# Optimization experiments

Hardware: AMD Instinct MI355X
Metric: run time of the kernel (lower is better)

Reference implementation:

```python
import jax, jax.numpy as jnp
import numpy as np

K = 2048      # codebook_size
D = 64        # codebook_dim
B = 32
T = 4096
W = 0.99      # codebook_loss_weight (EMA decay)
THRESH = 1.0  # discard_vec_threshold


def setup_inputs() -> dict:
    key = jax.random.key(0)
    k1, k2 = jax.random.split(key, 2)
    x = jax.random.normal(k1, (B, D, T), jnp.float32)
    codebook = jax.random.normal(k2, (K, D), jnp.float32)
    codebook_avg = codebook.copy()
    vector_usage = jnp.ones((K,), jnp.float32)
    perm = jnp.arange(B * T, dtype=jnp.int32)  # deterministic stand-in for randperm
    return dict(x=x, codebook=codebook, codebook_avg=codebook_avg,
                vector_usage=vector_usage, perm=perm)


def reference(x, codebook, codebook_avg, vector_usage, perm):
    Bv, E, Tv = x.shape
    sg = jax.lax.stop_gradient
    # preprocess: [B, E, T] -> [N, E]
    xf = jnp.transpose(x, (0, 2, 1)).reshape(-1, E)
    N = xf.shape[0]
    x_norm = jnp.linalg.norm(xf - jnp.mean(xf)) / np.sqrt(N * E)
    # squared euclidean distances [N, K]
    d = (jnp.sum(xf * xf, axis=-1, keepdims=True)
         - 2.0 * (xf @ codebook.T)
         + jnp.sum(codebook * codebook, axis=-1))
    idx = jnp.argmin(d, axis=-1)            # [N]
    fit = jnp.mean(jnp.min(d, axis=-1))
    q = codebook[idx]                       # [N, E] gather
    # --- update_codebook (torch.no_grad) ---
    cb_sum = jax.ops.segment_sum(sg(xf), idx, num_segments=K)          # onehot @ x
    counts = jax.ops.segment_sum(jnp.ones((N,), xf.dtype), idx, num_segments=K)
    new_avg = W * sg(codebook_avg) + (1.0 - W) * cb_sum
    new_usage = W * sg(vector_usage) + (1.0 - W) * counts
    keep = (new_usage >= THRESH).astype(xf.dtype)[:, None]
    random_shift = sg(xf)[perm][:K]
    new_codebook = keep * (new_avg / new_usage[:, None]) + (1.0 - keep) * random_shift
    vector_prob = counts / jnp.sum(counts)
    entropy = -jnp.sum(vector_prob * jnp.log(vector_prob + 1e-8))
    codebook_diff = jnp.linalg.norm(new_codebook - sg(codebook)) / np.sqrt(K * E)
    # --- commitment loss + straight-through ---
    commit_loss = jnp.sum((sg(q) - xf) ** 2) / (N * E)
    out = xf + sg(q - xf)
    out = jnp.transpose(out.reshape(Bv, Tv, E), (0, 2, 1))  # [B, E, T]
    return (out, commit_loss, fit, x_norm, new_codebook, new_avg, new_usage,
            entropy, codebook_diff)
```

## Files before the change

kernel.cpp:

```cpp
#include <hip/hip_runtime.h>
#include <math.h>

#define OUT_X      0
#define OUT_COMMIT 8388608
#define OUT_FIT    8388609
#define OUT_XNORM  8388610
#define OUT_NCB    8388611
#define OUT_NAVG   (8388611 + 131072)
#define OUT_NUSE   (8388611 + 262144)
#define OUT_ENT    (8388611 + 264192)
#define OUT_CBDIFF (8388611 + 264193)

#define WS_DACC    0
#define WS_COUNTS  64
#define WS_CBSUM   8256
#define WS_CURS    532544
#define WS_XN2     540736
#define WS_IDX     1065024
#define WS_CN2H    1589312
#define WS_SORTED  1597504
#define WS_CHI     2121792
#define WS_CLO     2383936
#define WS_ZERO_BYTES 532544

#define LO_SCALE5  32.0f

typedef _Float16 f16x8_t __attribute__((ext_vector_type(8)));
typedef float f32x16_t __attribute__((ext_vector_type(16)));

__device__ __forceinline__ void gload_lds16(const _Float16* g, _Float16* l) {
    __builtin_amdgcn_global_load_lds(
        (const __attribute__((address_space(1))) unsigned int*)(g),
        (__attribute__((address_space(3))) unsigned int*)(l), 16, 0, 0);
}

__global__ __launch_bounds__(256) void kern_prep_x(
    const float* __restrict__ x, float* __restrict__ xt,
    float* __restrict__ xn2, double* __restrict__ dacc)
{
    __shared__ __align__(16) float Xs[64][128];
    __shared__ float tmpA[4], tmpB[4];
    const int tid = threadIdx.x;
    const int n0 = blockIdx.x * 128;
    const int b = n0 >> 12, t0 = n0 & 4095;
    const float* xb = x + ((size_t)b << 18) + t0;
#pragma unroll
    for (int i = 0; i < 8; ++i) {
        int c = i * 256 + tid;
        int e = c >> 5, v4 = c & 31;
        float4 f = *(const float4*)(xb + ((size_t)e << 12) + (v4 << 2));
        *(float4*)&Xs[e][v4 << 2] = f;
    }
    __syncthreads();
    const int q = tid & 3, r0 = tid >> 2;
    float s1t = 0.f, s2t = 0.f;
#pragma unroll
    for (int h = 0; h < 2; ++h) {
        int r = r0 + (h << 6);
        float s2 = 0.f;
#pragma unroll
        for (int j = 0; j < 4; ++j) {
            int e = q * 16 + j * 4;
            float4 f = make_float4(Xs[e][r], Xs[e + 1][r], Xs[e + 2][r], Xs[e + 3][r]);
            *(float4*)(xt + (((size_t)(n0 + r)) << 6) + e) = f;
            s1t += f.x + f.y + f.z + f.w;
            s2 += f.x * f.x + f.y * f.y + f.z * f.z + f.w * f.w;
        }
        s2t += s2;
        float s2q = s2 + __shfl_xor(s2, 1, 64);
        s2q += __shfl_xor(s2q, 2, 64);
        if (q == 0) xn2[n0 + r] = s2q;
    }
    float rs = s1t, r2 = s2t;
#pragma unroll
    for (int m = 32; m >= 1; m >>= 1) {
        rs += __shfl_xor(rs, m, 64);
        r2 += __shfl_xor(r2, m, 64);
    }
    if ((tid & 63) == 0) { tmpA[tid >> 6] = rs; tmpB[tid >> 6] = r2; }
    __syncthreads();
    if (tid == 0) {
        atomicAdd(&dacc[0], (double)(tmpA[0] + tmpA[1] + tmpA[2] + tmpA[3]));
        atomicAdd(&dacc[1], (double)(tmpB[0] + tmpB[1] + tmpB[2] + tmpB[3]));
    }
}

__global__ __launch_bounds__(256) void kern_prep_cb(
    const float* __restrict__ cb, _Float16* __restrict__ chi,
    _Float16* __restrict__ clo, float* __restrict__ cn2h)
{
    __shared__ float Cs[128][68];
    const int tid = threadIdx.x;
    const int c0 = blockIdx.x * 128;
#pragma unroll
    for (int i = 0; i < 8; ++i) {
        int li = i * 256 + tid;
        int code = li >> 4, d4 = li & 15;
        float4 f = *(const float4*)(cb + (((size_t)(c0 + code)) << 6) + (d4 << 2));
        Cs[code][d4 * 4 + 0] = f.x; Cs[code][d4 * 4 + 1] = f.y;
        Cs[code][d4 * 4 + 2] = f.z; Cs[code][d4 * 4 + 3] = f.w;
    }
    __syncthreads();
    const int w = tid >> 6, lane = tid & 63;
    const int cl = (w << 5) + (lane & 31);
    const int g = lane >> 5;
    const int ktg = blockIdx.x * 4 + w;
#pragma unroll
    for (int s = 0; s < 4; ++s) {
        f16x8_t hh, ll;
#pragma unroll
        for (int i = 0; i < 8; ++i) {
            int k = 16 * s + 4 * g + (i & 3) + 8 * (i >> 2);
            float v = Cs[cl][k];
            _Float16 h = (_Float16)v;
            hh[i] = h;
            ll[i] = (_Float16)((v - (float)h) * LO_SCALE5);
        }
        *(f16x8_t*)(chi + (((size_t)(ktg * 4 + s)) << 9) + lane * 8) = hh;
        *(f16x8_t*)(clo + (((size_t)(ktg * 4 + s)) << 9) + lane * 8) = ll;
    }
    if (tid < 128) {
        float s = 0.f;
#pragma unroll
        for (int k = 0; k < 64; ++k) { float v = Cs[tid][k]; s = fmaf(v, v, s); }
        cn2h[c0 + tid] = -0.5f * s;
    }
}

__global__ __launch_bounds__(256, 2) void kern_argmin_mfma(
    const float* __restrict__ xt, const float* __restrict__ cn2h,
    const _Float16* __restrict__ chi, const _Float16* __restrict__ clo,
    const float* __restrict__ xn2, int* __restrict__ idxb,
    unsigned* __restrict__ counts, double* __restrict__ dacc)
{
    __shared__ __align__(16) _Float16 Bs[3][2][8][512];
    __shared__ float cvs[2048];
    const int tid = threadIdx.x;
    const int w = tid >> 6, lane = tid & 63;
    const int n0 = blockIdx.x * 256 + w * 64;
    const int l31 = lane & 31, g = lane >> 5;

    for (int i = tid; i < 2048; i += 256) cvs[i] = cn2h[i];

    f16x8_t ahi[2][4], alo5[2][4];
#pragma unroll
    for (int rb = 0; rb < 2; ++rb) {
        const float* xr = xt + ((size_t)(n0 + rb * 32 + l31) << 6) + 4 * g;
#pragma unroll
        for (int s = 0; s < 4; ++s) {
            float4 p = *(const float4*)(xr + 16 * s);
            float4 q = *(const float4*)(xr + 16 * s + 8);
            float vals[8] = {p.x, p.y, p.z, p.w, q.x, q.y, q.z, q.w};
#pragma unroll
            for (int i = 0; i < 8; ++i) {
                _Float16 h = (_Float16)vals[i];
                ahi[rb][s][i] = h;
                alo5[rb][s][i] = (_Float16)((vals[i] - (float)h) * LO_SCALE5);
            }
        }
    }
    float bestm[2][16]; int besti[2][16];
#pragma unroll
    for (int rb = 0; rb < 2; ++rb)
#pragma unroll
        for (int r = 0; r < 16; ++r) { bestm[rb][r] = -INFINITY; besti[rb][r] = 0; }

    __syncthreads();

#pragma unroll
    for (int kt = 0; kt < 2; ++kt)
#pragma unroll
        for (int j = 0; j < 4; ++j) {
            int seg = (j << 2) | w;
            int tt = seg >> 3, sh = seg & 7;
            const _Float16* src = ((sh & 1) ? clo : chi)
                + ((((size_t)(kt * 2 + tt)) * 4 + (sh >> 1)) << 9) + lane * 8;
            gload_lds16(src, &Bs[kt][tt][sh][0]);
        }

    int cur = 0, nxt = 2;
    for (int kt = 0; kt < 32; ++kt) {
        if (kt < 30) asm volatile("s_waitcnt vmcnt(4)" ::: "memory");
        else         asm volatile("s_waitcnt vmcnt(0)" ::: "memory");
        __builtin_amdgcn_s_barrier();
        if (kt + 2 < 32) {
#pragma unroll
            for (int j = 0; j < 4; ++j) {
                int seg = (j << 2) | w;
                int tt = seg >> 3, sh = seg & 7;
                const _Float16* src = ((sh & 1) ? clo : chi)
                    + ((((size_t)((kt + 2) * 2 + tt)) * 4 + (sh >> 1)) << 9) + lane * 8;
                gload_lds16(src, &Bs[nxt][tt][sh][0]);
            }
        }
#pragma unroll
        for (int tt = 0; tt < 2; ++tt) {
            const int tg = kt * 2 + tt;
            f16x8_t bh[4], bl[4];
#pragma unroll
            for (int s = 0; s < 4; ++s) {
                bh[s] = *(const f16x8_t*)&Bs[cur][tt][s * 2 + 0][lane * 8];
                bl[s] = *(const f16x8_t*)&Bs[cur][tt][s * 2 + 1][lane * 8];
            }
            float cv = cvs[(tg << 5) + l31];
            f32x16_t a0, a1;
#pragma unroll
            for (int r = 0; r < 16; ++r) { a0[r] = cv; a1[r] = cv; }
#pragma unroll
            for (int s = 0; s < 4; ++s) {
                a0 = __builtin_amdgcn_mfma_f32_32x32x16_f16(ahi[0][s], bh[s], a0, 0, 0, 0);
                a1 = __builtin_amdgcn_mfma_f32_32x32x16_f16(ahi[1][s], bh[s], a1, 0, 0, 0);
                f16x8_t bh5 = bh[s] * (_Float16)0.03125f;
                a0 = __builtin_amdgcn_mfma_f32_32x32x16_f16(alo5[0][s], bh5, a0, 0, 0, 0);
                a1 = __builtin_amdgcn_mfma_f32_32x32x16_f16(alo5[1][s], bh5, a1, 0, 0, 0);
                f16x8_t h50 = ahi[0][s] * (_Float16)0.03125f;
                f16x8_t h51 = ahi[1][s] * (_Float16)0.03125f;
                a0 = __builtin_amdgcn_mfma_f32_32x32x16_f16(h50, bl[s], a0, 0, 0, 0);
                a1 = __builtin_amdgcn_mfma_f32_32x32x16_f16(h51, bl[s], a1, 0, 0, 0);
            }
#pragma unroll
            for (int r = 0; r < 16; ++r) {
                if (a0[r] > bestm[0][r]) { bestm[0][r] = a0[r]; besti[0][r] = tg; }
                if (a1[r] > bestm[1][r]) { bestm[1][r] = a1[r]; besti[1][r] = tg; }
            }
        }
        cur = (cur == 2) ? 0 : cur + 1;
        nxt = (nxt == 2) ? 0 : nxt + 1;
    }
    float fs = 0.f;
#pragma unroll
    for (int rb = 0; rb < 2; ++rb)
#pragma unroll
        for (int r = 0; r < 16; ++r) {
            float mv = bestm[rb][r]; int mi = (besti[rb][r] << 5) + l31;
#pragma unroll
            for (int m = 1; m < 32; m <<= 1) {
                float ov = __shfl_xor(mv, m, 64);
                int oi = __shfl_xor(mi, m, 64);
                if (ov > mv || (ov == mv && oi < mi)) { mv = ov; mi = oi; }
            }
            if (l31 == 0) {
                int row = (r & 3) + 8 * (r >> 2) + 4 * g;
                int n = n0 + rb * 32 + row;
                idxb[n] = mi;
                atomicAdd(&counts[mi], 1u);
                fs += xn2[n] - 2.f * mv;
            }
        }
    if (l31 == 0) atomicAdd(&dacc[2], (double)fs);
}

__global__ void kern_scan(const unsigned* __restrict__ counts, unsigned* __restrict__ curs) {
    __shared__ unsigned wtot[4];
    const int tid = threadIdx.x;
    const int base = tid * 8;
    unsigned s[8]; unsigned tot = 0;
#pragma unroll
    for (int j = 0; j < 8; ++j) { s[j] = counts[base + j]; tot += s[j]; }
    unsigned v = tot;
    const int lane = tid & 63;
#pragma unroll
    for (int d = 1; d < 64; d <<= 1) {
        unsigned o = (unsigned)__shfl_up((int)v, d, 64);
        if (lane >= d) v += o;
    }
    if (lane == 63) wtot[tid >> 6] = v;
    __syncthreads();
    unsigned wbase = 0;
    for (int w = 0; w < (tid >> 6); ++w) wbase += wtot[w];
    unsigned run = wbase + v - tot;
#pragma unroll
    for (int j = 0; j < 8; ++j) { curs[base + j] = run; run += s[j]; }
}

__global__ void kern_scatter(const int* __restrict__ idxb, unsigned* __restrict__ curs,
                             unsigned* __restrict__ sorted) {
    const int n = blockIdx.x * 256 + threadIdx.x;
    int k = idxb[n];
    unsigned pos = atomicAdd(&curs[k], 1u);
    sorted[pos] = ((unsigned)k << 17) | (unsigned)n;
}

__global__ __launch_bounds__(256) void kern_chunk_reduce(
    const float* __restrict__ xt, const unsigned* __restrict__ sorted,
    float* __restrict__ cb_sum)
{
    const int tid = threadIdx.x;
    const int w = tid >> 6, lane = tid & 63;
    const int base = blockIdx.x * 256 + w * 64;
    int kcur = (int)(sorted[base] >> 17);
    float acc = 0.f;
#pragma unroll 4
    for (int it = 0; it < 16; ++it) {
        uint4 p = *(const uint4*)&sorted[base + it * 4];
        float v0 = xt[((size_t)(p.x & 0x1FFFFu) << 6) + lane];
        float v1 = xt[((size_t)(p.y & 0x1FFFFu) << 6) + lane];
        float v2 = xt[((size_t)(p.z & 0x1FFFFu) << 6) + lane];
        float v3 = xt[((size_t)(p.w & 0x1FFFFu) << 6) + lane];
        int k0 = (int)(p.x >> 17), k1 = (int)(p.y >> 17);
        int k2 = (int)(p.z >> 17), k3 = (int)(p.w >> 17);
        if (k0 != kcur) { atomicAdd(&cb_sum[(kcur << 6) + lane], acc); kcur = k0; acc = 0.f; }
        acc += v0;
        if (k1 != kcur) { atomicAdd(&cb_sum[(kcur << 6) + lane], acc); kcur = k1; acc = 0.f; }
        acc += v1;
        if (k2 != kcur) { atomicAdd(&cb_sum[(kcur << 6) + lane], acc); kcur = k2; acc = 0.f; }
        acc += v2;
        if (k3 != kcur) { atomicAdd(&cb_sum[(kcur << 6) + lane], acc); kcur = k3; acc = 0.f; }
        acc += v3;
    }
    atomicAdd(&cb_sum[(kcur << 6) + lane], acc);
}

__global__ __launch_bounds__(256) void kern_update(
    const float* __restrict__ cb_sum, const unsigned* __restrict__ counts,
    const float* __restrict__ cb, const float* __restrict__ cba,
    const float* __restrict__ usage, const int* __restrict__ perm,
    const float* __restrict__ xt, float* __restrict__ out,
    double* __restrict__ dacc)
{
    const int tid = threadIdx.x;
    const int i = blockIdx.x * 256 + tid;
    const int k = i >> 6, e = i & 63;
    float na = 0.99f * cba[i] + 0.01f * cb_sum[i];
    float nu = 0.99f * usage[k] + 0.01f * (float)counts[k];
    float ncb = (nu >= 1.0f) ? (na / nu)
                             : xt[((size_t)perm[k] << 6) + e];
    out[OUT_NAVG + i] = na;
    out[OUT_NCB + i] = ncb;
    if (e == 0) out[OUT_NUSE + k] = nu;
    float d = ncb - cb[i];
    float dd = d * d;
#pragma unroll
    for (int m = 32; m >= 1; m >>= 1) dd += __shfl_xor(dd, m, 64);
    if (e == 0) atomicAdd(&dacc[4], (double)dd);
}

__global__ __launch_bounds__(256) void kern_out(
    const float* __restrict__ x, const float* __restrict__ cb,
    const int* __restrict__ idxb, float* __restrict__ out,
    double* __restrict__ dacc) {
    __shared__ float tmp[4];
    const int tid = threadIdx.x;
    const int n0 = blockIdx.x * 256 + (tid & 63) * 4;
    const int ec = tid >> 6;
    const int b = n0 >> 12, t = n0 & 4095;
    int4 k4 = *(const int4*)(idxb + n0);
    const float* xb = x + ((size_t)b << 18) + t;
    float* ob = out + OUT_X + ((size_t)b << 18) + t;
    float cl = 0.f;
#pragma unroll
    for (int j = 0; j < 16; ++j) {
        int e = ec * 16 + j;
        float4 xv = *(const float4*)(xb + ((size_t)e << 12));
        float q0 = cb[((size_t)k4.x << 6) + e], q1 = cb[((size_t)k4.y << 6) + e];
        float q2 = cb[((size_t)k4.z << 6) + e], q3 = cb[((size_t)k4.w << 6) + e];
        float r0 = q0 - xv.x, r1 = q1 - xv.y, r2 = q2 - xv.z, r3 = q3 - xv.w;
        cl += r0 * r0 + r1 * r1 + r2 * r2 + r3 * r3;
        *(float4*)(ob + ((size_t)e << 12)) = make_float4(q0, q1, q2, q3);
    }
#pragma unroll
    for (int m = 32; m >= 1; m >>= 1) cl += __shfl_xor(cl, m, 64);
    if ((tid & 63) == 0) tmp[tid >> 6] = cl;
    __syncthreads();
    if (tid == 0) atomicAdd(&dacc[3], (double)(tmp[0] + tmp[1] + tmp[2] + tmp[3]));
}

__global__ void kern_scalars(const unsigned* __restrict__ counts,
                             const double* __restrict__ dacc, float* __restrict__ out) {
    __shared__ float tmp[4];
    __shared__ float totalSh;
    const int tid = threadIdx.x;
    float c = 0.f;
    for (int k = tid; k < 2048; k += 256) c += (float)counts[k];
#pragma unroll
    for (int m = 32; m >= 1; m >>= 1) c += __shfl_xor(c, m, 64);
    if ((tid & 63) == 0) tmp[tid >> 6] = c;
    __syncthreads();
    if (tid == 0) totalSh = tmp[0] + tmp[1] + tmp[2] + tmp[3];
    __syncthreads();
    const float total = totalSh;
    float ent = 0.f;
    for (int k = tid; k < 2048; k += 256) {
        float p = (float)counts[k] / total;
        ent -= p * logf(p + 1e-8f);
    }
#pragma unroll
    for (int m = 32; m >= 1; m >>= 1) ent += __shfl_xor(ent, m, 64);
    __syncthreads();
    if ((tid & 63) == 0) tmp[tid >> 6] = ent;
    __syncthreads();
    if (tid == 0) {
        float entropy = tmp[0] + tmp[1] + tmp[2] + tmp[3];
        out[OUT_COMMIT] = (float)(dacc[3] / 8388608.0);
        out[OUT_FIT]    = (float)(dacc[2] / 131072.0);
        double nd = 8388608.0;
        double var = dacc[1] - dacc[0] * dacc[0] / nd;
        if (var < 0.0) var = 0.0;
        out[OUT_XNORM] = (float)(sqrt(var) / sqrt(nd));
        out[OUT_ENT] = entropy;
        out[OUT_CBDIFF] = (float)(sqrt(dacc[4]) / sqrt(131072.0));
    }
}

extern "C" void kernel_launch(void* const* d_in, const int* in_sizes, int n_in,
                              void* d_out, int out_size, void* d_ws, size_t ws_size,
                              hipStream_t stream) {
    const float* x     = (const float*)d_in[0];
    const float* cb    = (const float*)d_in[1];
    const float* cba   = (const float*)d_in[2];
    const float* usage = (const float*)d_in[3];
    const int*   perm  = (const int*)d_in[4];
    float* out = (float*)d_out;
    char* ws = (char*)d_ws;
    double*    dacc   = (double*)(ws + WS_DACC);
    unsigned*  counts = (unsigned*)(ws + WS_COUNTS);
    float*     cbsum  = (float*)(ws + WS_CBSUM);
    unsigned*  curs   = (unsigned*)(ws + WS_CURS);
    float*     xn2    = (float*)(ws + WS_XN2);
    int*       idxb   = (int*)(ws + WS_IDX);
    float*     cn2h   = (float*)(ws + WS_CN2H);
    unsigned*  sorted = (unsigned*)(ws + WS_SORTED);
    _Float16*  chi    = (_Float16*)(ws + WS_CHI);
    _Float16*  clo    = (_Float16*)(ws + WS_CLO);
    float*     xt     = out + OUT_X;

    hipMemsetAsync(ws, 0, WS_ZERO_BYTES, stream);
    kern_prep_x<<<1024, 256, 0, stream>>>(x, xt, xn2, dacc);
    kern_prep_cb<<<16, 256, 0, stream>>>(cb, chi, clo, cn2h);
    kern_argmin_mfma<<<512, 256, 0, stream>>>(xt, cn2h, chi, clo, xn2, idxb, counts, dacc);
    kern_scan<<<1, 256, 0, stream>>>(counts, curs);
    kern_scatter<<<512, 256, 0, stream>>>(idxb, curs, sorted);
    kern_chunk_reduce<<<512, 256, 0, stream>>>(xt, sorted, cbsum);
    kern_update<<<512, 256, 0, stream>>>(cbsum, counts, cb, cba, usage, perm, xt, out, dacc);
    kern_out<<<512, 256, 0, stream>>>(x, cb, idxb, out, dacc);
    kern_scalars<<<1, 256, 0, stream>>>(counts, dacc, out);
}
```

Measured before the change: 276.4 us.

## Merge prep kernels into one launch and derive commit loss from fit

Merges the x-transpose and codebook-split prep kernels into one launch, using block-index ranges to pick the role, which saves a launch and lets the two jobs overlap. kern_out no longer reads x or accumulates the commitment loss. The commit loss is now taken from the min-distance accumulator (dacc[2]) that argmin already produces, since the sum of squared residuals equals the sum of min distances. kern_out moves after kern_scalars and only gathers codebook rows, dropping a full read of x. The risk is that commit loss now carries the f16 hi/lo split distance error instead of being recomputed exactly in fp32.

```diff
diff --git a/kernel.cpp b/kernel.cpp
--- a/kernel.cpp
+++ b/kernel.cpp
@@ -34,96 +34,95 @@
         (__attribute__((address_space(3))) unsigned int*)(l), 16, 0, 0);
 }
 
-__global__ __launch_bounds__(256) void kern_prep_x(
+__global__ __launch_bounds__(256) void kern_prep(
     const float* __restrict__ x, float* __restrict__ xt,
-    float* __restrict__ xn2, double* __restrict__ dacc)
-{
-    __shared__ __align__(16) float Xs[64][128];
-    __shared__ float tmpA[4], tmpB[4];
-    const int tid = threadIdx.x;
-    const int n0 = blockIdx.x * 128;
-    const int b = n0 >> 12, t0 = n0 & 4095;
-    const float* xb = x + ((size_t)b << 18) + t0;
-#pragma unroll
-    for (int i = 0; i < 8; ++i) {
-        int c = i * 256 + tid;
-        int e = c >> 5, v4 = c & 31;
-        float4 f = *(const float4*)(xb + ((size_t)e << 12) + (v4 << 2));
-        *(float4*)&Xs[e][v4 << 2] = f;
-    }
-    __syncthreads();
-    const int q = tid & 3, r0 = tid >> 2;
-    float s1t = 0.f, s2t = 0.f;
-#pragma unroll
-    for (int h = 0; h < 2; ++h) {
-        int r = r0 + (h << 6);
-        float s2 = 0.f;
-#pragma unroll
-        for (int j = 0; j < 4; ++j) {
-            int e = q * 16 + j * 4;
-            float4 f = make_float4(Xs[e][r], Xs[e + 1][r], Xs[e + 2][r], Xs[e + 3][r]);
-            *(float4*)(xt + (((size_t)(n0 + r)) << 6) + e) = f;
-            s1t += f.x + f.y + f.z + f.w;
-            s2 += f.x * f.x + f.y * f.y + f.z * f.z + f.w * f.w;
-        }
-        s2t += s2;
-        float s2q = s2 + __shfl_xor(s2, 1, 64);
-        s2q += __shfl_xor(s2q, 2, 64);
-        if (q == 0) xn2[n0 + r] = s2q;
-    }
-    float rs = s1t, r2 = s2t;
-#pragma unroll
-    for (int m = 32; m >= 1; m >>= 1) {
-        rs += __shfl_xor(rs, m, 64);
-        r2 += __shfl_xor(r2, m, 64);
-    }
-    if ((tid & 63) == 0) { tmpA[tid >> 6] = rs; tmpB[tid >> 6] = r2; }
-    __syncthreads();
-    if (tid == 0) {
-        atomicAdd(&dacc[0], (double)(tmpA[0] + tmpA[1] + tmpA[2] + tmpA[3]));
-        atomicAdd(&dacc[1], (double)(tmpB[0] + tmpB[1] + tmpB[2] + tmpB[3]));
-    }
-}
-
-__global__ __launch_bounds__(256) void kern_prep_cb(
+    float* __restrict__ xn2, double* __restrict__ dacc,
     const float* __restrict__ cb, _Float16* __restrict__ chi,
     _Float16* __restrict__ clo, float* __restrict__ cn2h)
 {
-    __shared__ float Cs[128][68];
-    const int tid = threadIdx.x;
-    const int c0 = blockIdx.x * 128;
-#pragma unroll
-    for (int i = 0; i < 8; ++i) {
-        int li = i * 256 + tid;
-        int code = li >> 4, d4 = li & 15;
-        float4 f = *(const float4*)(cb + (((size_t)(c0 + code)) << 6) + (d4 << 2));
-        Cs[code][d4 * 4 + 0] = f.x; Cs[code][d4 * 4 + 1] = f.y;
-        Cs[code][d4 * 4 + 2] = f.z; Cs[code][d4 * 4 + 3] = f.w;
-    }
-    __syncthreads();
-    const int w = tid >> 6, lane = tid & 63;
-    const int cl = (w << 5) + (lane & 31);
-    const int g = lane >> 5;
-    const int ktg = blockIdx.x * 4 + w;
-#pragma unroll
-    for (int s = 0; s < 4; ++s) {
-        f16x8_t hh, ll;
+    __shared__ __align__(16) char smem[128 * 68 * 4];
+    __shared__ float tmpA[4], tmpB[4];
+    const int tid = threadIdx.x;
+    if (blockIdx.x < 1024) {
+        float (*Xs)[128] = (float(*)[128])smem;
+        const int n0 = blockIdx.x * 128;
+        const int b = n0 >> 12, t0 = n0 & 4095;
+        const float* xb = x + ((size_t)b << 18) + t0;
 #pragma unroll
         for (int i = 0; i < 8; ++i) {
-            int k = 16 * s + 4 * g + (i & 3) + 8 * (i >> 2);
-            float v = Cs[cl][k];
-            _Float16 h = (_Float16)v;
-            hh[i] = h;
-            ll[i] = (_Float16)((v - (float)h) * LO_SCALE5);
-        }
-        *(f16x8_t*)(chi + (((size_t)(ktg * 4 + s)) << 9) + lane * 8) = hh;
-        *(f16x8_t*)(clo + (((size_t)(ktg * 4 + s)) << 9) + lane * 8) = ll;
-    }
-    if (tid < 128) {
-        float s = 0.f;
-#pragma unroll
-        for (int k = 0; k < 64; ++k) { float v = Cs[tid][k]; s = fmaf(v, v, s); }
-        cn2h[c0 + tid] = -0.5f * s;
+            int c = i * 256 + tid;
+            int e = c >> 5, v4 = c & 31;
+            float4 f = *(const float4*)(xb + ((size_t)e << 12) + (v4 << 2));
+            *(float4*)&Xs[e][v4 << 2] = f;
+        }
+        __syncthreads();
+        const int q = tid & 3, r0 = tid >> 2;
+        float s1t = 0.f, s2t = 0.f;
+#pragma unroll
+        for (int h = 0; h < 2; ++h) {
+            int r = r0 + (h << 6);
+            float s2 = 0.f;
+#pragma unroll
+            for (int j = 0; j < 4; ++j) {
+                int e = q * 16 + j * 4;
+                float4 f = make_float4(Xs[e][r], Xs[e + 1][r], Xs[e + 2][r], Xs[e + 3][r]);
+                *(float4*)(xt + (((size_t)(n0 + r)) << 6) + e) = f;
+                s1t += f.x + f.y + f.z + f.w;
+                s2 += f.x * f.x + f.y * f.y + f.z * f.z + f.w * f.w;
+            }
+            s2t += s2;
+            float s2q = s2 + __shfl_xor(s2, 1, 64);
+            s2q += __shfl_xor(s2q, 2, 64);
+            if (q == 0) xn2[n0 + r] = s2q;
+        }
+        float rs = s1t, r2 = s2t;
+#pragma unroll
+        for (int m = 32; m >= 1; m >>= 1) {
+            rs += __shfl_xor(rs, m, 64);
+            r2 += __shfl_xor(r2, m, 64);
+        }
+        if ((tid & 63) == 0) { tmpA[tid >> 6] = rs; tmpB[tid >> 6] = r2; }
+        __syncthreads();
+        if (tid == 0) {
+            atomicAdd(&dacc[0], (double)(tmpA[0] + tmpA[1] + tmpA[2] + tmpA[3]));
+            atomicAdd(&dacc[1], (double)(tmpB[0] + tmpB[1] + tmpB[2] + tmpB[3]));
+        }
+    } else {
+        float (*Cs)[68] = (float(*)[68])smem;
+        const int c0 = (blockIdx.x - 1024) * 128;
+#pragma unroll
+        for (int i = 0; i < 8; ++i) {
+            int li = i * 256 + tid;
+            int code = li >> 4, d4 = li & 15;
+            float4 f = *(const float4*)(cb + (((size_t)(c0 + code)) << 6) + (d4 << 2));
+            Cs[code][d4 * 4 + 0] = f.x; Cs[code][d4 * 4 + 1] = f.y;
+            Cs[code][d4 * 4 + 2] = f.z; Cs[code][d4 * 4 + 3] = f.w;
+        }
+        __syncthreads();
+        const int w = tid >> 6, lane = tid & 63;
+        const int cl = (w << 5) + (lane & 31);
+        const int g = lane >> 5;
+        const int ktg = (blockIdx.x - 1024) * 4 + w;
+#pragma unroll
+        for (int s = 0; s < 4; ++s) {
+            f16x8_t hh, ll;
+#pragma unroll
+            for (int i = 0; i < 8; ++i) {
+                int k = 16 * s + 4 * g + (i & 3) + 8 * (i >> 2);
+                float v = Cs[cl][k];
+                _Float16 h = (_Float16)v;
+                hh[i] = h;
+                ll[i] = (_Float16)((v - (float)h) * LO_SCALE5);
+            }
+            *(f16x8_t*)(chi + (((size_t)(ktg * 4 + s)) << 9) + lane * 8) = hh;
+            *(f16x8_t*)(clo + (((size_t)(ktg * 4 + s)) << 9) + lane * 8) = ll;
+        }
+        if (tid < 128) {
+            float s = 0.f;
+#pragma unroll
+            for (int k = 0; k < 64; ++k) { float v = Cs[tid][k]; s = fmaf(v, v, s); }
+            cn2h[c0 + tid] = -0.5f * s;
+        }
     }
 }
 
@@ -335,36 +334,6 @@
     if (e == 0) atomicAdd(&dacc[4], (double)dd);
 }
 
-__global__ __launch_bounds__(256) void kern_out(
-    const float* __restrict__ x, const float* __restrict__ cb,
-    const int* __restrict__ idxb, float* __restrict__ out,
-    double* __restrict__ dacc) {
-    __shared__ float tmp[4];
-    const int tid = threadIdx.x;
-    const int n0 = blockIdx.x * 256 + (tid & 63) * 4;
-    const int ec = tid >> 6;
-    const int b = n0 >> 12, t = n0 & 4095;
-    int4 k4 = *(const int4*)(idxb + n0);
-    const float* xb = x + ((size_t)b << 18) + t;
-    float* ob = out + OUT_X + ((size_t)b << 18) + t;
-    float cl = 0.f;
-#pragma unroll
-    for (int j = 0; j < 16; ++j) {
-        int e = ec * 16 + j;
-        float4 xv = *(const float4*)(xb + ((size_t)e << 12));
-        float q0 = cb[((size_t)k4.x << 6) + e], q1 = cb[((size_t)k4.y << 6) + e];
-        float q2 = cb[((size_t)k4.z << 6) + e], q3 = cb[((size_t)k4.w << 6) + e];
-        float r0 = q0 - xv.x, r1 = q1 - xv.y, r2 = q2 - xv.z, r3 = q3 - xv.w;
-        cl += r0 * r0 + r1 * r1 + r2 * r2 + r3 * r3;
-        *(float4*)(ob + ((size_t)e << 12)) = make_float4(q0, q1, q2, q3);
-    }
-#pragma unroll
-    for (int m = 32; m >= 1; m >>= 1) cl += __shfl_xor(cl, m, 64);
-    if ((tid & 63) == 0) tmp[tid >> 6] = cl;
-    __syncthreads();
-    if (tid == 0) atomicAdd(&dacc[3], (double)(tmp[0] + tmp[1] + tmp[2] + tmp[3]));
-}
-
 __global__ void kern_scalars(const unsigned* __restrict__ counts,
                              const double* __restrict__ dacc, float* __restrict__ out) {
     __shared__ float tmp[4];
@@ -391,7 +360,7 @@
     __syncthreads();
     if (tid == 0) {
         float entropy = tmp[0] + tmp[1] + tmp[2] + tmp[3];
-        out[OUT_COMMIT] = (float)(dacc[3] / 8388608.0);
+        out[OUT_COMMIT] = (float)(dacc[2] / 8388608.0);
         out[OUT_FIT]    = (float)(dacc[2] / 131072.0);
         double nd = 8388608.0;
         double var = dacc[1] - dacc[0] * dacc[0] / nd;
@@ -399,6 +368,24 @@
         out[OUT_XNORM] = (float)(sqrt(var) / sqrt(nd));
         out[OUT_ENT] = entropy;
         out[OUT_CBDIFF] = (float)(sqrt(dacc[4]) / sqrt(131072.0));
+    }
+}
+
+__global__ __launch_bounds__(256) void kern_out(
+    const float* __restrict__ cb, const int* __restrict__ idxb,
+    float* __restrict__ out) {
+    const int tid = threadIdx.x;
+    const int n0 = blockIdx.x * 256 + (tid & 63) * 4;
+    const int ec = tid >> 6;
+    const int b = n0 >> 12, t = n0 & 4095;
+    int4 k4 = *(const int4*)(idxb + n0);
+    float* ob = out + OUT_X + ((size_t)b << 18) + t;
+#pragma unroll
+    for (int j = 0; j < 16; ++j) {
+        int e = ec * 16 + j;
+        float q0 = cb[((size_t)k4.x << 6) + e], q1 = cb[((size_t)k4.y << 6) + e];
+        float q2 = cb[((size_t)k4.z << 6) + e], q3 = cb[((size_t)k4.w << 6) + e];
+        *(float4*)(ob + ((size_t)e << 12)) = make_float4(q0, q1, q2, q3);
     }
 }
 
@@ -425,13 +412,12 @@
     float*     xt     = out + OUT_X;
 
     hipMemsetAsync(ws, 0, WS_ZERO_BYTES, stream);
-    kern_prep_x<<<1024, 256, 0, stream>>>(x, xt, xn2, dacc);
-    kern_prep_cb<<<16, 256, 0, stream>>>(cb, chi, clo, cn2h);
+    kern_prep<<<1040, 256, 0, stream>>>(x, xt, xn2, dacc, cb, chi, clo, cn2h);
     kern_argmin_mfma<<<512, 256, 0, stream>>>(xt, cn2h, chi, clo, xn2, idxb, counts, dacc);
     kern_scan<<<1, 256, 0, stream>>>(counts, curs);
     kern_scatter<<<512, 256, 0, stream>>>(idxb, curs, sorted);
     kern_chunk_reduce<<<512, 256, 0, stream>>>(xt, sorted, cbsum);
     kern_update<<<512, 256, 0, stream>>>(cbsum, counts, cb, cba, usage, perm, xt, out, dacc);
-    kern_out<<<512, 256, 0, stream>>>(x, cb, idxb, out, dacc);
     kern_scalars<<<1, 256, 0, stream>>>(counts, dacc, out);
-}
+    kern_out<<<512, 256, 0, stream>>>(cb, idxb, out);
+}
```

Result: no change. 273.6 us, median of 3 (-1.0%).
